# Performance work log

Hardware: AMD Instinct MI355X
Metric: run time of the kernel (lower is better)

The kernel has to match this reference:

```python
import jax, jax.numpy as jnp
import numpy as np

B, INPUT_DIM, EMB_DIM = 16384, 2048, 768
DOMAIN_NUM, MEMORY_NUM, TAU = 9, 10, 32.0


def setup_inputs() -> dict:
    key = jax.random.key(0)
    k1, k2, k3, k4, k5 = jax.random.split(key, 5)
    feature = jax.random.normal(k1, (B, INPUT_DIM), dtype=jnp.float32)
    category = jax.random.randint(k2, (B,), 0, DOMAIN_NUM, dtype=jnp.int64)
    # Linear(input_dim, emb_dim, bias=False) weights: [emb_dim, input_dim]
    W_topic = jax.random.normal(k3, (EMB_DIM, INPUT_DIM), dtype=jnp.float32) * 0.02
    W_domain = jax.random.normal(k4, (EMB_DIM, INPUT_DIM), dtype=jnp.float32) * 0.02
    # domain_num Embedding(memory_num, emb_dim) tables, stacked: [D, M, E]
    memory_tables = jax.random.normal(k5, (DOMAIN_NUM, MEMORY_NUM, EMB_DIM), dtype=jnp.float32)
    return {"feature": feature, "W_topic": W_topic, "W_domain": W_domain,
            "memory_tables": memory_tables, "category": category}


def reference(feature, W_topic, W_domain, memory_tables, category):
    eps = 1e-12
    # F.normalize(feature, p=2, dim=-1)
    norm = jnp.maximum(jnp.linalg.norm(feature, axis=-1, keepdims=True), eps)
    feat = feature / norm                                   # [B, I]
    # per-sample gather of each sample's category memory table: [B, M, E]
    mem = memory_tables[category]
    # faithful quirk: loop over domain_num indexes the BATCH dim of the stack
    D = memory_tables.shape[0]
    mems_d = mem[:D]                                        # [D, M, E]
    t = feat @ W_topic.T                                    # [B, E]
    topic_att = jax.nn.softmax(jnp.einsum('be,dme->bdm', t, mems_d) * TAU, axis=-1)
    sep = jnp.einsum('bdm,dme->bde', topic_att, mems_d)     # [B, D, E]
    dproj = feat @ W_domain.T                               # [B, E]
    domain_att = jax.nn.softmax(jnp.einsum('bde,be->bd', sep, dproj) * TAU, axis=-1)
    return domain_att[:, None, :]                           # [B, 1, D]
```

## Files before the change

kernel.cpp:

```cpp
#include <hip/hip_runtime.h>
#include <math.h>

#define TAU_F 32.0f

typedef __attribute__((ext_vector_type(8))) _Float16 half8;
typedef __attribute__((ext_vector_type(2))) __fp16 half2v;
typedef __attribute__((ext_vector_type(4))) float f32x4;

union HU { uint4 u; half8 v; };

__device__ __forceinline__ void sync_lds_only() {
    asm volatile("s_waitcnt lgkmcnt(0)" ::: "memory");
    __builtin_amdgcn_s_barrier();
}

__global__ __launch_bounds__(256) void gproj2(
    const float* __restrict__ Wt, const float* __restrict__ Wd,
    const float* __restrict__ mem, const int* __restrict__ cat,
    float* __restrict__ P)
{
    __shared__ float Ml[96 * 36];
    __shared__ float Wl[32 * 68];

    const int bid = blockIdx.x;
    const int mat = bid >> 7;
    const int ks  = (bid >> 5) & 3;
    const int ct  = bid & 31;
    const int c0  = ct * 64;
    const int tid = threadIdx.x;
    const float* __restrict__ W = mat ? Wd : Wt;

    const int tr = tid >> 4;
    const int tc = tid & 15;

    float acc[6][4];
    #pragma unroll
    for (int j = 0; j < 6; ++j)
        #pragma unroll
        for (int q = 0; q < 4; ++q) acc[j][q] = 0.f;

    for (int ch = 0; ch < 6; ++ch) {
        __syncthreads();
        #pragma unroll
        for (int p = 0; p < 3; ++p) {
            const int idx = tid + 256 * p;
            const int r   = idx >> 3;
            const int kq  = idx & 7;
            float4 v = make_float4(0.f, 0.f, 0.f, 0.f);
            if (r < 90) {
                const int d = r / 10;
                const int mrow = cat[d] * 10 + (r - d * 10);
                v = *(const float4*)(mem + (size_t)mrow * 768 + ks * 192 + ch * 32 + kq * 4);
            }
            *(float4*)(Ml + r * 36 + kq * 4) = v;
        }
        #pragma unroll
        for (int p = 0; p < 2; ++p) {
            const int idx = tid + 256 * p;
            const int e   = idx >> 4;
            const int c4  = (idx & 15) * 4;
            *(float4*)(Wl + e * 68 + c4) =
                *(const float4*)(W + (size_t)(ks * 192 + ch * 32 + e) * 2048 + c0 + c4);
        }
        __syncthreads();

        #pragma unroll
        for (int e = 0; e < 32; e += 4) {
            float4 m4[6], w4[4];
            #pragma unroll
            for (int j = 0; j < 6; ++j) m4[j] = *(const float4*)(Ml + (tr * 6 + j) * 36 + e);
            #pragma unroll
            for (int q = 0; q < 4; ++q) w4[q] = *(const float4*)(Wl + (e + q) * 68 + tc * 4);
            #pragma unroll
            for (int j = 0; j < 6; ++j) {
                const float mv[4] = {m4[j].x, m4[j].y, m4[j].z, m4[j].w};
                #pragma unroll
                for (int q = 0; q < 4; ++q) {
                    acc[j][0] = fmaf(mv[q], w4[q].x, acc[j][0]);
                    acc[j][1] = fmaf(mv[q], w4[q].y, acc[j][1]);
                    acc[j][2] = fmaf(mv[q], w4[q].z, acc[j][2]);
                    acc[j][3] = fmaf(mv[q], w4[q].w, acc[j][3]);
                }
            }
        }
    }

    #pragma unroll
    for (int j = 0; j < 6; ++j) {
        float4 v = make_float4(acc[j][0], acc[j][1], acc[j][2], acc[j][3]);
        *(float4*)(P + (size_t)ks * 393216 + (size_t)(mat * 96 + tr * 6 + j) * 2048 + c0 + tc * 4) = v;
    }
}

__global__ __launch_bounds__(256) void split_g3(
    const float* __restrict__ P, unsigned short* __restrict__ gB)
{
    const int u  = blockIdx.x * 256 + threadIdx.x;
    const int n  = u >> 8;
    const int k0 = (u & 255) * 8;

    float s[8] = {0.f, 0.f, 0.f, 0.f, 0.f, 0.f, 0.f, 0.f};
    #pragma unroll
    for (int ks = 0; ks < 4; ++ks) {
        const float4 a = *(const float4*)(P + (size_t)ks * 393216 + (size_t)n * 2048 + k0);
        const float4 b = *(const float4*)(P + (size_t)ks * 393216 + (size_t)n * 2048 + k0 + 4);
        s[0] += a.x; s[1] += a.y; s[2] += a.z; s[3] += a.w;
        s[4] += b.x; s[5] += b.y; s[6] += b.z; s[7] += b.w;
    }
    union { _Float16 h[8]; uint4 u4; } hi, lo;
    #pragma unroll
    for (int e = 0; e < 8; ++e) {
        const _Float16 h = (_Float16)s[e];
        hi.h[e] = h;
        lo.h[e] = (_Float16)(s[e] - (float)h);
    }
    const int kc = k0 >> 5;
    const int lq = (k0 >> 3) & 3;
    const int nq = n / 48;
    const int rm = n - nq * 48;
    const int j  = rm >> 4;
    const int lm = rm & 15;
    const size_t fH = (size_t)((kc * 12 + nq * 3 + j) * 2 + 0) * 512 + lq * 128 + lm * 8;
    const size_t fL = (size_t)((kc * 12 + nq * 3 + j) * 2 + 1) * 512 + lq * 128 + lm * 8;
    *(uint4*)(gB + fH) = hi.u4;
    *(uint4*)(gB + fL) = lo.u4;
}

__global__ __launch_bounds__(512, 2) void fused_ep(
    const float* __restrict__ feat, const unsigned short* __restrict__ gB,
    float* __restrict__ out)
{
    __shared__ __align__(16) unsigned char smraw[114688];
    unsigned short* aS = (unsigned short*)smraw;
    unsigned short* Bl = (unsigned short*)(smraw + 40960);
    float* sc = (float*)smraw;
    __shared__ float ssqS[64];

    const int tid  = threadIdx.x;
    const int row0 = blockIdx.x * 64;

    const int w  = tid >> 6, l = tid & 63;
    const int lm = l & 15,  lq = l >> 4;
    const int iw = w >> 2;
    const int r  = w & 3;
    const bool roleT = (r < 2);
    const int f0 = 4 * r;
    const int tf = 2 + r;
    const int tp = 2 * tf;
    const int dp = 12 + 3 * (r - 2);
    const int db = 6 + 3 * (r - 2);
    const int sr = tid >> 3, kq = tid & 7;
    const int skf = kq >> 2, sk4 = kq & 3;

    f32x4 acc[2][4];
    #pragma unroll
    for (int i = 0; i < 2; ++i)
        #pragma unroll
        for (int j = 0; j < 4; ++j) acc[i][j] = (f32x4)0.f;
    float ssq = 0.f;

    const float* fbase = feat + (size_t)(row0 + sr) * 2048 + kq * 8;

    auto loadB = [&](int kt2, uint4* bn) {
        #pragma unroll
        for (int s = 0; s < 5; ++s) {
            const int p = w + 8 * s;
            if (p < 36) {
                const int kf = (p >= 18) ? 1 : 0;
                const int fi = p - kf * 18;
                const int cf = (fi < 12) ? (fi >> 1) : (fi - 6);
                const int pl = (fi < 12) ? (fi & 1) : 0;
                bn[s] = *(const uint4*)(gB + (size_t)(((2 * kt2 + kf) * 12 + cf) * 1024)
                                           + pl * 512 + l * 8);
            }
        }
    };
    auto writeB = [&](int buf, const uint4* bn) {
        #pragma unroll
        for (int s = 0; s < 5; ++s) {
            const int p = w + 8 * s;
            if (p < 36)
                *(uint4*)(Bl + ((size_t)buf * 36 + p) * 512 + l * 8) = bn[s];
        }
    };

    auto cw = [&](int buf, float4 va, float4 vb) {
        const float xs[8] = {va.x, va.y, va.z, va.w, vb.x, vb.y, vb.z, vb.w};
        union { half2v h2[4]; uint4 u4; } uh, ul;
        #pragma unroll
        for (int e = 0; e < 4; ++e) {
            const float a = xs[2 * e], b = xs[2 * e + 1];
            ssq = fmaf(a, a, ssq); ssq = fmaf(b, b, ssq);
            half2v h = __builtin_amdgcn_cvt_pkrtz(a, b);
            uh.h2[e] = h;
            ul.h2[e] = __builtin_amdgcn_cvt_pkrtz(a - (float)h[0], b - (float)h[1]);
        }
        *(uint4*)(aS + (size_t)(((buf * 2 + 0) * 2 + skf) * 64 + sr) * 40 + sk4 * 8) = uh.u4;
        *(uint4*)(aS + (size_t)(((buf * 2 + 1) * 2 + skf) * 64 + sr) * 40 + sk4 * 8) = ul.u4;
    };

    {
        uint4 b0[5];
        loadB(0, b0);
        float4 c0a = *(const float4*)(fbase);
        float4 c0b = *(const float4*)(fbase + 4);
        cw(0, c0a, c0b);
        writeB(0, b0);
    }
    float4 c1a = *(const float4*)(fbase + 64);
    float4 c1b = *(const float4*)(fbase + 68);
    sync_lds_only();

    for (int kt = 0; kt < 32; ++kt) {
        const int cb = kt & 1;
        uint4 bn[5];
        if (kt < 31) loadB(kt + 1, bn);
        const int ka = (kt + 2 < 32) ? kt + 2 : 31;
        float4 cna = *(const float4*)(fbase + ka * 64);
        float4 cnb = *(const float4*)(fbase + ka * 64 + 4);
        if (kt < 31) cw((kt + 1) & 1, c1a, c1b);

        half8 fh[2][2], fl[2][2];
        #pragma unroll
        for (int ii = 0; ii < 2; ++ii)
            #pragma unroll
            for (int kf = 0; kf < 2; ++kf) {
                const int row = (iw * 2 + ii) * 16 + lm;
                HU th, tl;
                th.u = *(const uint4*)(aS + (size_t)(((cb * 2 + 0) * 2 + kf) * 64 + row) * 40 + lq * 8);
                tl.u = *(const uint4*)(aS + (size_t)(((cb * 2 + 1) * 2 + kf) * 64 + row) * 40 + lq * 8);
                fh[ii][kf] = th.v;
                fl[ii][kf] = tl.v;
            }

        if (roleT) {
            #pragma unroll
            for (int kf = 0; kf < 2; ++kf) {
                const unsigned short* bp = Bl + ((size_t)cb * 36 + kf * 18) * 512 + l * 8;
                HU hA, hB, hC, hD;
                hA.u = *(const uint4*)(bp + (size_t)(f0 + 0) * 512);
                hB.u = *(const uint4*)(bp + (size_t)(f0 + 1) * 512);
                hC.u = *(const uint4*)(bp + (size_t)(f0 + 2) * 512);
                hD.u = *(const uint4*)(bp + (size_t)(f0 + 3) * 512);
                #pragma unroll
                for (int ii = 0; ii < 2; ++ii) {
                    acc[ii][0] = __builtin_amdgcn_mfma_f32_16x16x32_f16(fh[ii][kf], hA.v, acc[ii][0], 0, 0, 0);
                    acc[ii][0] = __builtin_amdgcn_mfma_f32_16x16x32_f16(fh[ii][kf], hB.v, acc[ii][0], 0, 0, 0);
                    acc[ii][0] = __builtin_amdgcn_mfma_f32_16x16x32_f16(fl[ii][kf], hA.v, acc[ii][0], 0, 0, 0);
                    acc[ii][1] = __builtin_amdgcn_mfma_f32_16x16x32_f16(fh[ii][kf], hC.v, acc[ii][1], 0, 0, 0);
                    acc[ii][1] = __builtin_amdgcn_mfma_f32_16x16x32_f16(fh[ii][kf], hD.v, acc[ii][1], 0, 0, 0);
                    acc[ii][1] = __builtin_amdgcn_mfma_f32_16x16x32_f16(fl[ii][kf], hC.v, acc[ii][1], 0, 0, 0);
                }
            }
        } else {
            #pragma unroll
            for (int kf = 0; kf < 2; ++kf) {
                const unsigned short* bp = Bl + ((size_t)cb * 36 + kf * 18) * 512 + l * 8;
                HU hA, hB, hC, hD, hE;
                hA.u = *(const uint4*)(bp + (size_t)(tp + 0) * 512);
                hB.u = *(const uint4*)(bp + (size_t)(tp + 1) * 512);
                hC.u = *(const uint4*)(bp + (size_t)(dp + 0) * 512);
                hD.u = *(const uint4*)(bp + (size_t)(dp + 1) * 512);
                hE.u = *(const uint4*)(bp + (size_t)(dp + 2) * 512);
                #pragma unroll
                for (int ii = 0; ii < 2; ++ii) {
                    acc[ii][0] = __builtin_amdgcn_mfma_f32_16x16x32_f16(fh[ii][kf], hA.v, acc[ii][0], 0, 0, 0);
                    acc[ii][0] = __builtin_amdgcn_mfma_f32_16x16x32_f16(fh[ii][kf], hB.v, acc[ii][0], 0, 0, 0);
                    acc[ii][0] = __builtin_amdgcn_mfma_f32_16x16x32_f16(fl[ii][kf], hA.v, acc[ii][0], 0, 0, 0);
                    acc[ii][1] = __builtin_amdgcn_mfma_f32_16x16x32_f16(fh[ii][kf], hC.v, acc[ii][1], 0, 0, 0);
                    acc[ii][2] = __builtin_amdgcn_mfma_f32_16x16x32_f16(fh[ii][kf], hD.v, acc[ii][2], 0, 0, 0);
                    acc[ii][3] = __builtin_amdgcn_mfma_f32_16x16x32_f16(fh[ii][kf], hE.v, acc[ii][3], 0, 0, 0);
                }
            }
        }

        if (kt < 31) writeB((kt + 1) & 1, bn);

        sync_lds_only();
        c1a = cna; c1b = cnb;
    }

    if (roleT) {
        #pragma unroll
        for (int ii = 0; ii < 2; ++ii)
            #pragma unroll
            for (int f = 0; f < 2; ++f)
                #pragma unroll
                for (int r4 = 0; r4 < 4; ++r4)
                    sc[((iw * 2 + ii) * 16 + lq * 4 + r4) * 193 + (2 * r + f) * 16 + lm] = acc[ii][f][r4];
    } else {
        #pragma unroll
        for (int ii = 0; ii < 2; ++ii)
            #pragma unroll
            for (int f = 0; f < 4; ++f) {
                const int cf = (f == 0) ? tf : (db + f - 1);
                #pragma unroll
                for (int r4 = 0; r4 < 4; ++r4)
                    sc[((iw * 2 + ii) * 16 + lq * 4 + r4) * 193 + cf * 16 + lm] = acc[ii][f][r4];
            }
    }

    ssq += __shfl_xor(ssq, 1, 64);
    ssq += __shfl_xor(ssq, 2, 64);
    ssq += __shfl_xor(ssq, 4, 64);
    if (kq == 0) ssqS[sr] = ssq;
    __syncthreads();

    if (tid < 128) {
        const int rr = tid >> 1, hf = tid & 1;
        const int nd = hf ? 4 : 5;
        const int d0 = hf ? 5 : 0;
        const float inv = TAU_F / fmaxf(sqrtf(ssqS[rr]), 1e-12f);
        const float* scr = sc + (size_t)rr * 193;
        float lg[5];
        float dmax = -1e30f;
        #pragma unroll
        for (int dd = 0; dd < 5; ++dd) {
            if (dd < nd) {
                const int d = d0 + dd;
                const float* v = scr + d * 10;
                const float* u = scr + 96 + d * 10;
                float mx = v[0];
                #pragma unroll
                for (int m = 1; m < 10; ++m) mx = fmaxf(mx, v[m]);
                float ssum = 0.f, dot = 0.f;
                #pragma unroll
                for (int m = 0; m < 10; ++m) {
                    const float p = __expf((v[m] - mx) * inv);
                    ssum += p;
                    dot = fmaf(p, u[m], dot);
                }
                const float lgt = (dot / ssum) * inv;
                lg[dd] = lgt;
                dmax = fmaxf(dmax, lgt);
            } else {
                lg[dd] = -1e30f;
            }
        }
        dmax = fmaxf(dmax, __shfl_xor(dmax, 1, 64));
        float s2 = 0.f;
        #pragma unroll
        for (int dd = 0; dd < 5; ++dd) {
            const float p = __expf(lg[dd] - dmax);
            lg[dd] = p;
            s2 += p;
        }
        s2 += __shfl_xor(s2, 1, 64);
        const float r2 = 1.0f / s2;
        #pragma unroll
        for (int dd = 0; dd < 5; ++dd)
            if (dd < nd)
                out[(size_t)(row0 + rr) * 9 + d0 + dd] = lg[dd] * r2;
    }
}

extern "C" void kernel_launch(void* const* d_in, const int* in_sizes, int n_in,
                              void* d_out, int out_size, void* d_ws, size_t ws_size,
                              hipStream_t stream) {
    const float* feature = (const float*)d_in[0];
    const float* Wt      = (const float*)d_in[1];
    const float* Wd      = (const float*)d_in[2];
    const float* mem     = (const float*)d_in[3];
    const int*   cat     = (const int*)d_in[4];

    float* P  = (float*)d_ws;
    unsigned short* gB = (unsigned short*)((char*)d_ws + 50331648);
    float* out = (float*)d_out;

    gproj2<<<256, 256, 0, stream>>>(Wt, Wd, mem, cat, P);
    split_g3<<<192, 256, 0, stream>>>(P, gB);
    fused_ep<<<256, 512, 0, stream>>>(feature, gB, out);
}
```

Measured before the change: 261.7 us.

## Load GEMM operands directly into registers, dropping LDS staging and barriers

```diff
diff --git a/kernel.cpp b/kernel.cpp
--- a/kernel.cpp
+++ b/kernel.cpp
@@ -8,11 +8,6 @@
 typedef __attribute__((ext_vector_type(4))) float f32x4;
 
 union HU { uint4 u; half8 v; };
-
-__device__ __forceinline__ void sync_lds_only() {
-    asm volatile("s_waitcnt lgkmcnt(0)" ::: "memory");
-    __builtin_amdgcn_s_barrier();
-}
 
 __global__ __launch_bounds__(256) void gproj2(
     const float* __restrict__ Wt, const float* __restrict__ Wd,
@@ -130,10 +125,7 @@
     const float* __restrict__ feat, const unsigned short* __restrict__ gB,
     float* __restrict__ out)
 {
-    __shared__ __align__(16) unsigned char smraw[114688];
-    unsigned short* aS = (unsigned short*)smraw;
-    unsigned short* Bl = (unsigned short*)(smraw + 40960);
-    float* sc = (float*)smraw;
+    __shared__ float sc[64 * 193];
     __shared__ float ssqS[64];
 
     const int tid  = threadIdx.x;
@@ -141,107 +133,87 @@
 
     const int w  = tid >> 6, l = tid & 63;
     const int lm = l & 15,  lq = l >> 4;
-    const int iw = w >> 2;
+    const int half = w >> 2;
     const int r  = w & 3;
     const bool roleT = (r < 2);
-    const int f0 = 4 * r;
-    const int tf = 2 + r;
-    const int tp = 2 * tf;
-    const int dp = 12 + 3 * (r - 2);
-    const int db = 6 + 3 * (r - 2);
-    const int sr = tid >> 3, kq = tid & 7;
-    const int skf = kq >> 2, sk4 = kq & 3;
+    const int cf0 = 2 * r;
+    const int tf  = 2 + r;
+    const int db  = 6 + 3 * (r - 2);
 
     f32x4 acc[2][4];
     #pragma unroll
     for (int i = 0; i < 2; ++i)
         #pragma unroll
         for (int j = 0; j < 4; ++j) acc[i][j] = (f32x4)0.f;
-    float ssq = 0.f;
-
-    const float* fbase = feat + (size_t)(row0 + sr) * 2048 + kq * 8;
-
-    auto loadB = [&](int kt2, uint4* bn) {
-        #pragma unroll
-        for (int s = 0; s < 5; ++s) {
-            const int p = w + 8 * s;
-            if (p < 36) {
-                const int kf = (p >= 18) ? 1 : 0;
-                const int fi = p - kf * 18;
-                const int cf = (fi < 12) ? (fi >> 1) : (fi - 6);
-                const int pl = (fi < 12) ? (fi & 1) : 0;
-                bn[s] = *(const uint4*)(gB + (size_t)(((2 * kt2 + kf) * 12 + cf) * 1024)
-                                           + pl * 512 + l * 8);
-            }
-        }
+    float ssq0 = 0.f, ssq1 = 0.f;
+
+    const float* abase = feat + (size_t)(row0 + half * 32 + lm) * 2048 + lq * 8;
+    const unsigned short* lB = gB + l * 8;
+
+    auto loadA = [&](int kt, float4 a[2][2][2]) {
+        #pragma unroll
+        for (int ii = 0; ii < 2; ++ii)
+            #pragma unroll
+            for (int kf = 0; kf < 2; ++kf) {
+                const float* p = abase + (size_t)ii * 16 * 2048 + kt * 64 + kf * 32;
+                a[ii][kf][0] = *(const float4*)(p);
+                a[ii][kf][1] = *(const float4*)(p + 4);
+            }
     };
-    auto writeB = [&](int buf, const uint4* bn) {
-        #pragma unroll
-        for (int s = 0; s < 5; ++s) {
-            const int p = w + 8 * s;
-            if (p < 36)
-                *(uint4*)(Bl + ((size_t)buf * 36 + p) * 512 + l * 8) = bn[s];
+    auto loadB = [&](int kt, uint4 b[2][5]) {
+        #pragma unroll
+        for (int kf = 0; kf < 2; ++kf) {
+            if (roleT) {
+                const unsigned short* p = lB + (size_t)((2 * kt + kf) * 12 + cf0) * 1024;
+                b[kf][0] = *(const uint4*)(p);
+                b[kf][1] = *(const uint4*)(p + 512);
+                b[kf][2] = *(const uint4*)(p + 1024);
+                b[kf][3] = *(const uint4*)(p + 1536);
+            } else {
+                const unsigned short* pt = lB + (size_t)((2 * kt + kf) * 12 + tf) * 1024;
+                b[kf][0] = *(const uint4*)(pt);
+                b[kf][1] = *(const uint4*)(pt + 512);
+                const unsigned short* pd = lB + (size_t)((2 * kt + kf) * 12 + db) * 1024;
+                b[kf][2] = *(const uint4*)(pd);
+                b[kf][3] = *(const uint4*)(pd + 1024);
+                b[kf][4] = *(const uint4*)(pd + 2048);
+            }
         }
     };
-
-    auto cw = [&](int buf, float4 va, float4 vb) {
+    auto conv8 = [](float4 va, float4 vb, half8& oh, half8& ol, float& s) {
         const float xs[8] = {va.x, va.y, va.z, va.w, vb.x, vb.y, vb.z, vb.w};
-        union { half2v h2[4]; uint4 u4; } uh, ul;
+        union { half2v h2[4]; half8 v; } uh, ul;
         #pragma unroll
         for (int e = 0; e < 4; ++e) {
             const float a = xs[2 * e], b = xs[2 * e + 1];
-            ssq = fmaf(a, a, ssq); ssq = fmaf(b, b, ssq);
+            s = fmaf(a, a, s); s = fmaf(b, b, s);
             half2v h = __builtin_amdgcn_cvt_pkrtz(a, b);
             uh.h2[e] = h;
             ul.h2[e] = __builtin_amdgcn_cvt_pkrtz(a - (float)h[0], b - (float)h[1]);
         }
-        *(uint4*)(aS + (size_t)(((buf * 2 + 0) * 2 + skf) * 64 + sr) * 40 + sk4 * 8) = uh.u4;
-        *(uint4*)(aS + (size_t)(((buf * 2 + 1) * 2 + skf) * 64 + sr) * 40 + sk4 * 8) = ul.u4;
+        oh = uh.v; ol = ul.v;
     };
 
-    {
-        uint4 b0[5];
-        loadB(0, b0);
-        float4 c0a = *(const float4*)(fbase);
-        float4 c0b = *(const float4*)(fbase + 4);
-        cw(0, c0a, c0b);
-        writeB(0, b0);
-    }
-    float4 c1a = *(const float4*)(fbase + 64);
-    float4 c1b = *(const float4*)(fbase + 68);
-    sync_lds_only();
+    float4 a0[2][2][2], a1[2][2][2];
+    uint4  b0[2][5],    b1[2][5];
+    loadA(0, a0);
+    loadB(0, b0);
 
     for (int kt = 0; kt < 32; ++kt) {
-        const int cb = kt & 1;
-        uint4 bn[5];
-        if (kt < 31) loadB(kt + 1, bn);
-        const int ka = (kt + 2 < 32) ? kt + 2 : 31;
-        float4 cna = *(const float4*)(fbase + ka * 64);
-        float4 cnb = *(const float4*)(fbase + ka * 64 + 4);
-        if (kt < 31) cw((kt + 1) & 1, c1a, c1b);
+        if (kt < 31) { loadA(kt + 1, a1); loadB(kt + 1, b1); }
 
         half8 fh[2][2], fl[2][2];
         #pragma unroll
-        for (int ii = 0; ii < 2; ++ii)
+        for (int ii = 0; ii < 2; ++ii) {
+            conv8(a0[ii][0][0], a0[ii][0][1], fh[ii][0], fl[ii][0], ii ? ssq1 : ssq0);
+            conv8(a0[ii][1][0], a0[ii][1][1], fh[ii][1], fl[ii][1], ii ? ssq1 : ssq0);
+        }
+
+        if (roleT) {
             #pragma unroll
             for (int kf = 0; kf < 2; ++kf) {
-                const int row = (iw * 2 + ii) * 16 + lm;
-                HU th, tl;
-                th.u = *(const uint4*)(aS + (size_t)(((cb * 2 + 0) * 2 + kf) * 64 + row) * 40 + lq * 8);
-                tl.u = *(const uint4*)(aS + (size_t)(((cb * 2 + 1) * 2 + kf) * 64 + row) * 40 + lq * 8);
-                fh[ii][kf] = th.v;
-                fl[ii][kf] = tl.v;
-            }
-
-        if (roleT) {
-            #pragma unroll
-            for (int kf = 0; kf < 2; ++kf) {
-                const unsigned short* bp = Bl + ((size_t)cb * 36 + kf * 18) * 512 + l * 8;
                 HU hA, hB, hC, hD;
-                hA.u = *(const uint4*)(bp + (size_t)(f0 + 0) * 512);
-                hB.u = *(const uint4*)(bp + (size_t)(f0 + 1) * 512);
-                hC.u = *(const uint4*)(bp + (size_t)(f0 + 2) * 512);
-                hD.u = *(const uint4*)(bp + (size_t)(f0 + 3) * 512);
+                hA.u = b0[kf][0]; hB.u = b0[kf][1]; hC.u = b0[kf][2]; hD.u = b0[kf][3];
                 #pragma unroll
                 for (int ii = 0; ii < 2; ++ii) {
                     acc[ii][0] = __builtin_amdgcn_mfma_f32_16x16x32_f16(fh[ii][kf], hA.v, acc[ii][0], 0, 0, 0);
@@ -255,13 +227,9 @@
         } else {
             #pragma unroll
             for (int kf = 0; kf < 2; ++kf) {
-                const unsigned short* bp = Bl + ((size_t)cb * 36 + kf * 18) * 512 + l * 8;
                 HU hA, hB, hC, hD, hE;
-                hA.u = *(const uint4*)(bp + (size_t)(tp + 0) * 512);
-                hB.u = *(const uint4*)(bp + (size_t)(tp + 1) * 512);
-                hC.u = *(const uint4*)(bp + (size_t)(dp + 0) * 512);
-                hD.u = *(const uint4*)(bp + (size_t)(dp + 1) * 512);
-                hE.u = *(const uint4*)(bp + (size_t)(dp + 2) * 512);
+                hA.u = b0[kf][0]; hB.u = b0[kf][1]; hC.u = b0[kf][2];
+                hD.u = b0[kf][3]; hE.u = b0[kf][4];
                 #pragma unroll
                 for (int ii = 0; ii < 2; ++ii) {
                     acc[ii][0] = __builtin_amdgcn_mfma_f32_16x16x32_f16(fh[ii][kf], hA.v, acc[ii][0], 0, 0, 0);
@@ -274,10 +242,17 @@
             }
         }
 
-        if (kt < 31) writeB((kt + 1) & 1, bn);
-
-        sync_lds_only();
-        c1a = cna; c1b = cnb;
+        #pragma unroll
+        for (int ii = 0; ii < 2; ++ii)
+            #pragma unroll
+            for (int kf = 0; kf < 2; ++kf) {
+                a0[ii][kf][0] = a1[ii][kf][0];
+                a0[ii][kf][1] = a1[ii][kf][1];
+            }
+        #pragma unroll
+        for (int kf = 0; kf < 2; ++kf)
+            #pragma unroll
+            for (int q = 0; q < 5; ++q) b0[kf][q] = b1[kf][q];
     }
 
     if (roleT) {
@@ -287,7 +262,7 @@
             for (int f = 0; f < 2; ++f)
                 #pragma unroll
                 for (int r4 = 0; r4 < 4; ++r4)
-                    sc[((iw * 2 + ii) * 16 + lq * 4 + r4) * 193 + (2 * r + f) * 16 + lm] = acc[ii][f][r4];
+                    sc[(half * 32 + ii * 16 + lq * 4 + r4) * 193 + (cf0 + f) * 16 + lm] = acc[ii][f][r4];
     } else {
         #pragma unroll
         for (int ii = 0; ii < 2; ++ii)
@@ -296,14 +271,18 @@
                 const int cf = (f == 0) ? tf : (db + f - 1);
                 #pragma unroll
                 for (int r4 = 0; r4 < 4; ++r4)
-                    sc[((iw * 2 + ii) * 16 + lq * 4 + r4) * 193 + cf * 16 + lm] = acc[ii][f][r4];
-            }
-    }
-
-    ssq += __shfl_xor(ssq, 1, 64);
-    ssq += __shfl_xor(ssq, 2, 64);
-    ssq += __shfl_xor(ssq, 4, 64);
-    if (kq == 0) ssqS[sr] = ssq;
+                    sc[(half * 32 + ii * 16 + lq * 4 + r4) * 193 + cf * 16 + lm] = acc[ii][f][r4];
+            }
+    }
+
+    ssq0 += __shfl_xor(ssq0, 16, 64);
+    ssq0 += __shfl_xor(ssq0, 32, 64);
+    ssq1 += __shfl_xor(ssq1, 16, 64);
+    ssq1 += __shfl_xor(ssq1, 32, 64);
+    if (r == 0 && l < 16) {
+        ssqS[half * 32 + lm]      = ssq0;
+        ssqS[half * 32 + 16 + lm] = ssq1;
+    }
     __syncthreads();
 
     if (tid < 128) {
```

Measured after the change: 678.6 us. 2.59x slower.
